# Performance work log

Measured on AMD Instinct MI355X. Metric: run time of the kernel, lower is better.

## Reference

```python
import jax, jax.numpy as jnp
import numpy as np

N = 100_000   # nodes
E = 1_600_000 # edges (avg degree 16)
IN, H, C = 3, 32, 4
DIMS = [(IN, H), (H, 2 * H), (2 * H, 3 * H), (3 * H, 4 * H)]  # SAGEConv layer dims


def setup_inputs() -> dict:
    key = jax.random.key(0)
    ks = jax.random.split(key, 16)
    inp = {
        "x": jax.random.normal(ks[0], (N, IN), dtype=jnp.float32),
        "edge_index": jax.random.randint(ks[1], (2, E), 0, N, dtype=jnp.int32).astype(jnp.int64),
    }
    i = 2
    for l, (din, dout) in enumerate(DIMS):
        s = 1.0 / float(np.sqrt(din))
        inp[f"Wl{l}"] = jax.random.normal(ks[i], (din, dout), dtype=jnp.float32) * s; i += 1
        inp[f"bl{l}"] = jnp.zeros((dout,), jnp.float32)
        inp[f"Wr{l}"] = jax.random.normal(ks[i], (din, dout), dtype=jnp.float32) * s; i += 1
    sf = 1.0 / float(np.sqrt(4 * H))
    inp["Wf"] = jax.random.normal(ks[i], (4 * H, C), dtype=jnp.float32) * sf
    inp["bf"] = jnp.zeros((C,), jnp.float32)
    return inp


def _sage_conv(h, src, dst, Wl, bl, Wr):
    # PyG SAGEConv (aggr='mean'): lin_l(mean_{j in N(i)} x_j) + lin_r(x_i)
    n = h.shape[0]
    agg = jax.ops.segment_sum(h[src], dst, num_segments=n)            # [N, din]
    deg = jax.ops.segment_sum(jnp.ones((src.shape[0],), h.dtype), dst, num_segments=n)
    mean = agg / jnp.maximum(deg, 1.0)[:, None]
    return mean @ Wl + bl + h @ Wr


def reference(x, edge_index, Wl0, bl0, Wr0, Wl1, bl1, Wr1, Wl2, bl2, Wr2, Wl3, bl3, Wr3, Wf, bf):
    src, dst = edge_index[0], edge_index[1]
    h = x
    for Wl, bl, Wr in ((Wl0, bl0, Wr0), (Wl1, bl1, Wr1), (Wl2, bl2, Wr2), (Wl3, bl3, Wr3)):
        h = jax.nn.relu(_sage_conv(h, src, dst, Wl, bl, Wr))
    return jax.nn.sigmoid(h @ Wf + bf)  # [N, class_num]
```

## Files before the change

### kernel.cpp

```cpp
#include <hip/hip_runtime.h>
#include <math.h>

#define NN 100000
#define NE 1600000
#define BUCKETS ((NN + 255) >> 8)
#define RTH 1024
#define RVPT 4

typedef short bf16x8 __attribute__((ext_vector_type(8)));
typedef float f32x4 __attribute__((ext_vector_type(4)));

__device__ inline float bsf(unsigned short u) { return __uint_as_float(((unsigned)u) << 16); }
__device__ inline unsigned short f2bs(float f) {
    unsigned u = __float_as_uint(f);
    return (unsigned short)((u + 0x7fffu + ((u >> 16) & 1u)) >> 16);
}

__global__ __launch_bounds__(RTH) void bhist_k(const int* __restrict__ dst,
                                               int* __restrict__ bhist) {
    __shared__ int bh[BUCKETS];
    for (int i = threadIdx.x; i < BUCKETS; i += RTH) bh[i] = 0;
    __syncthreads();
    int e0 = blockIdx.x * (RTH * RVPT) + threadIdx.x;
#pragma unroll
    for (int v = 0; v < RVPT; ++v) {
        int e = e0 + v * RTH;
        if (e < NE) atomicAdd(&bh[dst[e] >> 8], 1);
    }
    __syncthreads();
    for (int i = threadIdx.x; i < BUCKETS; i += RTH)
        if (bh[i]) atomicAdd(&bhist[i], bh[i]);
}

__global__ __launch_bounds__(512) void bscan_k(const int* __restrict__ bhist,
                                               int* __restrict__ bcur) {
    __shared__ int buf[512];
    int tid = threadIdx.x;
    int v = (tid < BUCKETS) ? bhist[tid] : 0;
    buf[tid] = v;
    __syncthreads();
    for (int off = 1; off < 512; off <<= 1) {
        int t = (tid >= off) ? buf[tid - off] : 0;
        __syncthreads();
        buf[tid] += t;
        __syncthreads();
    }
    if (tid < BUCKETS) bcur[tid] = buf[tid] - v;
}

__global__ __launch_bounds__(RTH) void reorder_k(const int* __restrict__ src,
                                                 const int* __restrict__ dst,
                                                 int* __restrict__ bcur,
                                                 unsigned long long* __restrict__ ebuf) {
    __shared__ int hist[BUCKETS];
    __shared__ int base[BUCKETS];
    int tid = threadIdx.x;
    for (int i = tid; i < BUCKETS; i += RTH) hist[i] = 0;
    __syncthreads();
    int e0 = blockIdx.x * (RTH * RVPT) + tid;
    unsigned long long pair[RVPT];
    int pr[RVPT];
#pragma unroll
    for (int v = 0; v < RVPT; ++v) {
        int e = e0 + v * RTH;
        if (e < NE) {
            int s = src[e], d = dst[e];
            pair[v] = ((unsigned long long)(unsigned)d << 32) | (unsigned)s;
            int b = d >> 8;
            int r = atomicAdd(&hist[b], 1);
            pr[v] = (b << 12) | r;
        } else pr[v] = -1;
    }
    __syncthreads();
    for (int i = tid; i < BUCKETS; i += RTH)
        base[i] = hist[i] ? atomicAdd(&bcur[i], hist[i]) : 0;
    __syncthreads();
#pragma unroll
    for (int v = 0; v < RVPT; ++v) {
        if (pr[v] >= 0) {
            int b = pr[v] >> 12, r = pr[v] & 4095;
            ebuf[(size_t)base[b] + r] = pair[v];
        }
    }
}

__global__ __launch_bounds__(512) void pcsr_k(const unsigned long long* __restrict__ ebuf,
                                              const int* __restrict__ bend,
                                              int* __restrict__ row_ptr,
                                              int* __restrict__ col) {
    __shared__ int hist[256];
    __shared__ int wsum[4];
    int b = blockIdx.x;
    int tid = threadIdx.x;
    int beg = b ? bend[b - 1] : 0;
    int end = bend[b];

    if (tid < 256) hist[tid] = 0;
    __syncthreads();
    for (int e = beg + tid; e < end; e += 512)
        atomicAdd(&hist[(int)(ebuf[e] >> 32) & 255], 1);
    __syncthreads();

    int v = 0, excl = 0;
    if (tid < 256) {
        v = hist[tid];
        int lane = tid & 63, wid = tid >> 6;
        int s = v;
#pragma unroll
        for (int off = 1; off < 64; off <<= 1) {
            int t = __shfl_up(s, off);
            if (lane >= off) s += t;
        }
        if (lane == 63) wsum[wid] = s;
        excl = s - v;
    }
    __syncthreads();
    if (tid < 256) {
        int wid = tid >> 6;
        int prev = 0;
#pragma unroll
        for (int w = 0; w < 4; ++w) prev += (w < wid) ? wsum[w] : 0;
        excl += beg + prev;
        int node = b * 256 + tid;
        if (node < NN) row_ptr[node] = excl;
        if (node == NN - 1) row_ptr[NN] = excl + v;
    }
    __syncthreads();
    if (tid < 256) hist[tid] = excl;
    __syncthreads();
    for (int e = beg + tid; e < end; e += 512) {
        unsigned long long p = ebuf[e];
        int d = (int)(p >> 32);
        int pos = atomicAdd(&hist[d & 255], 1);
        col[pos] = (int)(p & 0xffffffffu);
    }
}

__global__ __launch_bounds__(256) void wcvt_all_k(
    const float* __restrict__ Wl1, const float* __restrict__ Wr1,
    const float* __restrict__ Wl2, const float* __restrict__ Wr2,
    const float* __restrict__ Wl3, const float* __restrict__ Wr3,
    unsigned short* __restrict__ wt1, unsigned short* __restrict__ wt2,
    unsigned short* __restrict__ wt3) {
    int idx = blockIdx.x * 256 + threadIdx.x;
    if (idx < 4096) {
        int j = idx >> 6, k = idx & 63;
        float v = (k < 32) ? Wl1[k * 64 + j] : Wr1[(k - 32) * 64 + j];
        wt1[idx] = f2bs(v);
    } else if (idx < 16384) {
        int t = idx - 4096;
        int j = t / 128, k = t - j * 128;
        float v = (k < 64) ? Wl2[k * 96 + j] : Wr2[(k - 64) * 96 + j];
        wt2[t] = f2bs(v);
    } else if (idx < 40960) {
        int t = idx - 16384;
        int j = t / 192, k = t - j * 192;
        float v = (k < 96) ? Wl3[k * 128 + j] : Wr3[(k - 96) * 128 + j];
        wt3[t] = f2bs(v);
    }
}

__global__ __launch_bounds__(256) void agg0_k(const int* __restrict__ rp, const int* __restrict__ col,
                                              const float* __restrict__ x, unsigned short* __restrict__ magg) {
    int node = blockIdx.x * 4 + (threadIdx.x >> 6);
    int lane = threadIdx.x & 63;
    int fl = lane & 3, es = lane >> 2;
    int beg = rp[node], end = rp[node + 1];
    float acc = 0.0f;
    for (int e = beg + es; e < end; e += 16) {
        unsigned off = (unsigned)(col[e] * 3);
        if (fl < 3) acc += x[off + fl];
    }
    acc += __shfl(acc, lane + 32);
    acc += __shfl(acc, lane + 16);
    acc += __shfl(acc, lane + 8);
    acc += __shfl(acc, lane + 4);
    if (lane < 3) {
        float inv = 1.0f / fmaxf((float)(end - beg), 1.0f);
        magg[(size_t)node * 3 + lane] = f2bs(acc * inv);
    }
}

template<int DIN, int FL, int EPW>
__global__ __launch_bounds__(256) void agg_k(const int* __restrict__ rp, const int* __restrict__ col,
                                             const unsigned short* __restrict__ hb,
                                             unsigned short* __restrict__ magg) {
    int node = blockIdx.x * 4 + (threadIdx.x >> 6);
    int lane = threadIdx.x & 63;
    int fl = lane % FL;
    int es = lane / FL;
    int beg = rp[node], end = rp[node + 1];

    float a[8];
#pragma unroll
    for (int i = 0; i < 8; ++i) a[i] = 0.0f;

    if (es < EPW) {
        for (int e = beg + es; e < end; e += 4 * EPW) {
            int e1 = e + EPW, e2 = e + 2 * EPW, e3 = e + 3 * EPW;
            bool b1 = e1 < end, b2 = e2 < end, b3 = e3 < end;
            unsigned o0 = (unsigned)(col[e] * DIN);
            unsigned o1 = (unsigned)(col[b1 ? e1 : e] * DIN);
            unsigned o2 = (unsigned)(col[b2 ? e2 : e] * DIN);
            unsigned o3 = (unsigned)(col[b3 ? e3 : e] * DIN);
            uint4 v0 = *(const uint4*)(hb + o0 + fl * 8);
            uint4 v1 = *(const uint4*)(hb + o1 + fl * 8);
            uint4 v2 = *(const uint4*)(hb + o2 + fl * 8);
            uint4 v3 = *(const uint4*)(hb + o3 + fl * 8);
            float m1 = b1 ? 1.0f : 0.0f;
            float m2 = b2 ? 1.0f : 0.0f;
            float m3 = b3 ? 1.0f : 0.0f;
            const unsigned short* p0 = (const unsigned short*)&v0;
            const unsigned short* p1 = (const unsigned short*)&v1;
            const unsigned short* p2 = (const unsigned short*)&v2;
            const unsigned short* p3 = (const unsigned short*)&v3;
#pragma unroll
            for (int i = 0; i < 8; ++i) {
                a[i] += bsf(p0[i]);
                a[i] = fmaf(bsf(p1[i]), m1, a[i]);
                a[i] = fmaf(bsf(p2[i]), m2, a[i]);
                a[i] = fmaf(bsf(p3[i]), m3, a[i]);
            }
        }
    }

    if constexpr (FL == 4) {
#pragma unroll
        for (int i = 0; i < 8; ++i) {
            a[i] += __shfl(a[i], lane + 4);
            a[i] += __shfl(a[i], lane + 8);
            a[i] += __shfl(a[i], lane + 16);
            a[i] += __shfl(a[i], lane + 32);
        }
    } else if constexpr (FL == 8) {
#pragma unroll
        for (int i = 0; i < 8; ++i) {
            a[i] += __shfl(a[i], lane + 8);
            a[i] += __shfl(a[i], lane + 16);
            a[i] += __shfl(a[i], lane + 32);
        }
    } else {
#pragma unroll
        for (int i = 0; i < 8; ++i) {
            float g4 = __shfl(a[i], lane + 48);
            a[i] += __shfl(a[i], lane + 12);
            a[i] += __shfl(a[i], lane + 24);
            a[i] += g4;
        }
    }

    if (lane < FL) {
        float inv = 1.0f / fmaxf((float)(end - beg), 1.0f);
        unsigned short o[8];
#pragma unroll
        for (int i = 0; i < 8; ++i) o[i] = f2bs(a[i] * inv);
        *(uint4*)(magg + (size_t)node * DIN + fl * 8) = *(const uint4*)o;
    }
}

template<int DIN, int DOUT, int CT>
__global__ __launch_bounds__(256) void gemm_k(
    const unsigned short* __restrict__ magg, const float* __restrict__ hx,
    const float* __restrict__ Wl, const float* __restrict__ bl, const float* __restrict__ Wr,
    unsigned short* __restrict__ hout)
{
    __shared__ float sm[32][DIN + 1];
    __shared__ float sh[32][DIN + 1];

    int tx = threadIdx.x;
    int base = blockIdx.x * 32;

    for (int f = tx; f < 32 * 3; f += 256) {
        int n = f / 3, k = f - n * 3;
        sm[n][k] = bsf(magg[(size_t)(base + n) * 3 + k]);
        sh[n][k] = hx[(size_t)(base + n) * 3 + k];
    }
    __syncthreads();

    int ng = tx >> 5, cg = tx & 31;
    float acc[4][CT];
#pragma unroll
    for (int m = 0; m < 4; ++m)
#pragma unroll
        for (int c = 0; c < CT; ++c) acc[m][c] = bl[cg * CT + c];

#pragma unroll
    for (int k = 0; k < 3; ++k) {
        float wl[CT], wr[CT];
#pragma unroll
        for (int c = 0; c < CT; ++c) {
            wl[c] = Wl[(size_t)k * DOUT + cg * CT + c];
            wr[c] = Wr[(size_t)k * DOUT + cg * CT + c];
        }
#pragma unroll
        for (int m = 0; m < 4; ++m) {
            float mv = sm[ng * 4 + m][k];
            float hv = sh[ng * 4 + m][k];
#pragma unroll
            for (int c = 0; c < CT; ++c)
                acc[m][c] = fmaf(mv, wl[c], fmaf(hv, wr[c], acc[m][c]));
        }
    }

#pragma unroll
    for (int m = 0; m < 4; ++m)
#pragma unroll
        for (int c = 0; c < CT; ++c) {
            float v = fmaxf(acc[m][c], 0.0f);
            hout[(size_t)(base + ng * 4 + m) * DOUT + cg * CT + c] = f2bs(v);
        }
}

template<int DIN, int DOUT, bool FINAL>
__global__ __launch_bounds__(256) void mgemm_k(
    const unsigned short* __restrict__ magg, const unsigned short* __restrict__ h,
    const unsigned short* __restrict__ Wt, const float* __restrict__ bl,
    const float* __restrict__ Wf, const float* __restrict__ bfi,
    unsigned short* __restrict__ hout, float* __restrict__ out)
{
    constexpr int K2  = 2 * DIN;
    constexpr int STR = K2 + 8;
    constexpr int NT  = DOUT / 16;
    constexpr int KS  = K2 / 32;
    __shared__ unsigned short lA[64 * STR];
    __shared__ unsigned short lB[DOUT * STR];

    int tx = threadIdx.x;
    int base = blockIdx.x * 64;

    constexpr int CPM = DIN / 8;
    for (int c = tx; c < 64 * CPM; c += 256) {
        int n = c / CPM, o = (c - n * CPM) * 8;
        int node = base + n;
        uint4 vm = make_uint4(0, 0, 0, 0), vh = vm;
        if (node < NN) {
            vm = *(const uint4*)(magg + (size_t)node * DIN + o);
            vh = *(const uint4*)(h    + (size_t)node * DIN + o);
        }
        *(uint4*)(lA + n * STR + o)       = vm;
        *(uint4*)(lA + n * STR + DIN + o) = vh;
    }
    constexpr int CPW = K2 / 8;
    for (int c = tx; c < DOUT * CPW; c += 256) {
        int j = c / CPW, o = (c - j * CPW) * 8;
        *(uint4*)(lB + j * STR + o) = *(const uint4*)(Wt + (size_t)j * K2 + o);
    }
    __syncthreads();

    int lane = tx & 63;
    int wm = tx >> 6;
    int r16 = lane & 15, kg = lane >> 4;

    f32x4 acc[NT];
#pragma unroll
    for (int t = 0; t < NT; ++t) acc[t] = (f32x4){0.0f, 0.0f, 0.0f, 0.0f};

#pragma unroll
    for (int kk = 0; kk < KS; ++kk) {
        bf16x8 a = *(const bf16x8*)(lA + (wm * 16 + r16) * STR + kk * 32 + kg * 8);
#pragma unroll
        for (int t = 0; t < NT; ++t) {
            bf16x8 b = *(const bf16x8*)(lB + (t * 16 + r16) * STR + kk * 32 + kg * 8);
            acc[t] = __builtin_amdgcn_mfma_f32_16x16x32_bf16(a, b, acc[t], 0, 0, 0);
        }
    }

    if (!FINAL) {
#pragma unroll
        for (int t = 0; t < NT; ++t)
#pragma unroll
            for (int r = 0; r < 4; ++r) {
                int node = base + wm * 16 + kg * 4 + r;
                int colj = t * 16 + r16;
                float v = fmaxf(acc[t][r] + bl[colj], 0.0f);
                if (node < NN) hout[(size_t)node * DOUT + colj] = f2bs(v);
            }
    } else {
        __syncthreads();
        float* s4 = (float*)lB;
#pragma unroll
        for (int t = 0; t < NT; ++t)
#pragma unroll
            for (int r = 0; r < 4; ++r) {
                int nl = wm * 16 + kg * 4 + r;
                int colj = t * 16 + r16;
                s4[nl * 129 + colj] = fmaxf(acc[t][r] + bl[colj], 0.0f);
            }
        __syncthreads();
        int nl = tx >> 2, c = tx & 3;
        int node = base + nl;
        if (node < NN) {
            float a = bfi[c];
#pragma unroll 8
            for (int k = 0; k < 128; ++k)
                a = fmaf(s4[nl * 129 + k], Wf[k * 4 + c], a);
            out[(size_t)node * 4 + c] = 1.0f / (1.0f + expf(-a));
        }
    }
}

extern "C" void kernel_launch(void* const* d_in, const int* in_sizes, int n_in,
                              void* d_out, int out_size, void* d_ws, size_t ws_size,
                              hipStream_t stream) {
    const float* x   = (const float*)d_in[0];
    const int*   ei  = (const int*)d_in[1];
    const int*   src = ei;
    const int*   dst = ei + NE;
    const float* Wl0 = (const float*)d_in[2];
    const float* bl0 = (const float*)d_in[3];
    const float* Wr0 = (const float*)d_in[4];
    const float* Wl1 = (const float*)d_in[5];
    const float* bl1 = (const float*)d_in[6];
    const float* Wr1 = (const float*)d_in[7];
    const float* Wl2 = (const float*)d_in[8];
    const float* bl2 = (const float*)d_in[9];
    const float* Wr2 = (const float*)d_in[10];
    const float* Wl3 = (const float*)d_in[11];
    const float* bl3 = (const float*)d_in[12];
    const float* Wr3 = (const float*)d_in[13];
    const float* Wf  = (const float*)d_in[14];
    const float* bf  = (const float*)d_in[15];
    float* out = (float*)d_out;

    size_t ints = (size_t)(NN + 2) + 512 + 512 + NE;
    ints = (ints + 15) & ~(size_t)15;
    size_t need = ints * 4 + (size_t)NN * (96 + 32 + 64 + 96) * 2
                + (size_t)(64 * 64 + 96 * 128 + 128 * 192) * 2;
    if (ws_size < need) return;

    int* row_ptr = (int*)d_ws;
    int* bhist   = row_ptr + NN + 2;
    int* bcur    = bhist + 512;
    int* col     = bcur + 512;
    unsigned short* magg = (unsigned short*)((char*)d_ws + ints * 4);
    unsigned long long* ebuf = (unsigned long long*)magg;
    unsigned short* h1   = magg + (size_t)NN * 96;
    unsigned short* h2   = h1 + (size_t)NN * 32;
    unsigned short* h3   = h2 + (size_t)NN * 64;
    unsigned short* wt1  = h3 + (size_t)NN * 96;
    unsigned short* wt2  = wt1 + 64 * 64;
    unsigned short* wt3  = wt2 + 96 * 128;

    wcvt_all_k<<<160, 256, 0, stream>>>(Wl1, Wr1, Wl2, Wr2, Wl3, Wr3, wt1, wt2, wt3);

    hipMemsetAsync(bhist, 0, 512 * sizeof(int), stream);
    const int EB = (NE + RTH * RVPT - 1) / (RTH * RVPT);
    bhist_k<<<EB, RTH, 0, stream>>>(dst, bhist);
    bscan_k<<<1, 512, 0, stream>>>(bhist, bcur);
    reorder_k<<<EB, RTH, 0, stream>>>(src, dst, bcur, ebuf);
    pcsr_k<<<BUCKETS, 512, 0, stream>>>(ebuf, bcur, row_ptr, col);

    const int AGRID = NN / 4;
    const int MG    = (NN + 63) / 64;

    agg0_k<<<AGRID, 256, 0, stream>>>(row_ptr, col, x, magg);
    gemm_k<3, 32, 1><<<NN / 32, 256, 0, stream>>>(magg, x, Wl0, bl0, Wr0, h1);

    agg_k<32, 4, 16><<<AGRID, 256, 0, stream>>>(row_ptr, col, h1, magg);
    mgemm_k<32, 64, false><<<MG, 256, 0, stream>>>(
        magg, h1, wt1, bl1, nullptr, nullptr, h2, nullptr);

    agg_k<64, 8, 8><<<AGRID, 256, 0, stream>>>(row_ptr, col, h2, magg);
    mgemm_k<64, 96, false><<<MG, 256, 0, stream>>>(
        magg, h2, wt2, bl2, nullptr, nullptr, h3, nullptr);

    agg_k<96, 12, 5><<<AGRID, 256, 0, stream>>>(row_ptr, col, h3, magg);
    mgemm_k<96, 128, true><<<MG, 256, 0, stream>>>(
        magg, h3, wt3, bl3, Wf, bf, nullptr, out);
}
```

Baseline: 289.1 us.

## Fuse neighbor aggregation into MFMA GEMM kernels and reduce final layer in registers

Merges the per-layer mean-aggregation kernel into the MFMA GEMM kernel, so each block aggregates its 64 nodes straight into shared memory. This removes the aggregated-feature round trip through global memory and one launch per layer. Weight tiles are no longer staged in LDS but read from global memory (cache) inside the MFMA loop. The final classifier is now reduced with cross-lane shuffles instead of an LDS pass. The risk is lower parallelism: each wave now walks 16 nodes serially, and the grid shrinks from 25000 blocks to about 1563.

Result: slower. 341.5 us (+18.1%).

```diff
diff --git a/kernel.cpp b/kernel.cpp
--- a/kernel.cpp
+++ b/kernel.cpp
@@ -181,83 +181,6 @@
     }
 }
 
-template<int DIN, int FL, int EPW>
-__global__ __launch_bounds__(256) void agg_k(const int* __restrict__ rp, const int* __restrict__ col,
-                                             const unsigned short* __restrict__ hb,
-                                             unsigned short* __restrict__ magg) {
-    int node = blockIdx.x * 4 + (threadIdx.x >> 6);
-    int lane = threadIdx.x & 63;
-    int fl = lane % FL;
-    int es = lane / FL;
-    int beg = rp[node], end = rp[node + 1];
-
-    float a[8];
-#pragma unroll
-    for (int i = 0; i < 8; ++i) a[i] = 0.0f;
-
-    if (es < EPW) {
-        for (int e = beg + es; e < end; e += 4 * EPW) {
-            int e1 = e + EPW, e2 = e + 2 * EPW, e3 = e + 3 * EPW;
-            bool b1 = e1 < end, b2 = e2 < end, b3 = e3 < end;
-            unsigned o0 = (unsigned)(col[e] * DIN);
-            unsigned o1 = (unsigned)(col[b1 ? e1 : e] * DIN);
-            unsigned o2 = (unsigned)(col[b2 ? e2 : e] * DIN);
-            unsigned o3 = (unsigned)(col[b3 ? e3 : e] * DIN);
-            uint4 v0 = *(const uint4*)(hb + o0 + fl * 8);
-            uint4 v1 = *(const uint4*)(hb + o1 + fl * 8);
-            uint4 v2 = *(const uint4*)(hb + o2 + fl * 8);
-            uint4 v3 = *(const uint4*)(hb + o3 + fl * 8);
-            float m1 = b1 ? 1.0f : 0.0f;
-            float m2 = b2 ? 1.0f : 0.0f;
-            float m3 = b3 ? 1.0f : 0.0f;
-            const unsigned short* p0 = (const unsigned short*)&v0;
-            const unsigned short* p1 = (const unsigned short*)&v1;
-            const unsigned short* p2 = (const unsigned short*)&v2;
-            const unsigned short* p3 = (const unsigned short*)&v3;
-#pragma unroll
-            for (int i = 0; i < 8; ++i) {
-                a[i] += bsf(p0[i]);
-                a[i] = fmaf(bsf(p1[i]), m1, a[i]);
-                a[i] = fmaf(bsf(p2[i]), m2, a[i]);
-                a[i] = fmaf(bsf(p3[i]), m3, a[i]);
-            }
-        }
-    }
-
-    if constexpr (FL == 4) {
-#pragma unroll
-        for (int i = 0; i < 8; ++i) {
-            a[i] += __shfl(a[i], lane + 4);
-            a[i] += __shfl(a[i], lane + 8);
-            a[i] += __shfl(a[i], lane + 16);
-            a[i] += __shfl(a[i], lane + 32);
-        }
-    } else if constexpr (FL == 8) {
-#pragma unroll
-        for (int i = 0; i < 8; ++i) {
-            a[i] += __shfl(a[i], lane + 8);
-            a[i] += __shfl(a[i], lane + 16);
-            a[i] += __shfl(a[i], lane + 32);
-        }
-    } else {
-#pragma unroll
-        for (int i = 0; i < 8; ++i) {
-            float g4 = __shfl(a[i], lane + 48);
-            a[i] += __shfl(a[i], lane + 12);
-            a[i] += __shfl(a[i], lane + 24);
-            a[i] += g4;
-        }
-    }
-
-    if (lane < FL) {
-        float inv = 1.0f / fmaxf((float)(end - beg), 1.0f);
-        unsigned short o[8];
-#pragma unroll
-        for (int i = 0; i < 8; ++i) o[i] = f2bs(a[i] * inv);
-        *(uint4*)(magg + (size_t)node * DIN + fl * 8) = *(const uint4*)o;
-    }
-}
-
 template<int DIN, int DOUT, int CT>
 __global__ __launch_bounds__(256) void gemm_k(
     const unsigned short* __restrict__ magg, const float* __restrict__ hx,
@@ -312,8 +235,9 @@
 }
 
 template<int DIN, int DOUT, bool FINAL>
-__global__ __launch_bounds__(256) void mgemm_k(
-    const unsigned short* __restrict__ magg, const unsigned short* __restrict__ h,
+__global__ __launch_bounds__(256) void fused_k(
+    const int* __restrict__ rp, const int* __restrict__ col,
+    const unsigned short* __restrict__ h,
     const unsigned short* __restrict__ Wt, const float* __restrict__ bl,
     const float* __restrict__ Wf, const float* __restrict__ bfi,
     unsigned short* __restrict__ hout, float* __restrict__ out)
@@ -322,33 +246,100 @@
     constexpr int STR = K2 + 8;
     constexpr int NT  = DOUT / 16;
     constexpr int KS  = K2 / 32;
+    constexpr int FL  = DIN / 8;
+    constexpr int EPW = 64 / FL;
     __shared__ unsigned short lA[64 * STR];
-    __shared__ unsigned short lB[DOUT * STR];
 
     int tx = threadIdx.x;
+    int lane = tx & 63;
+    int wm = tx >> 6;
     int base = blockIdx.x * 64;
 
     constexpr int CPM = DIN / 8;
     for (int c = tx; c < 64 * CPM; c += 256) {
         int n = c / CPM, o = (c - n * CPM) * 8;
         int node = base + n;
-        uint4 vm = make_uint4(0, 0, 0, 0), vh = vm;
-        if (node < NN) {
-            vm = *(const uint4*)(magg + (size_t)node * DIN + o);
-            vh = *(const uint4*)(h    + (size_t)node * DIN + o);
-        }
-        *(uint4*)(lA + n * STR + o)       = vm;
+        uint4 vh = make_uint4(0, 0, 0, 0);
+        if (node < NN) vh = *(const uint4*)(h + (size_t)node * DIN + o);
         *(uint4*)(lA + n * STR + DIN + o) = vh;
     }
-    constexpr int CPW = K2 / 8;
-    for (int c = tx; c < DOUT * CPW; c += 256) {
-        int j = c / CPW, o = (c - j * CPW) * 8;
-        *(uint4*)(lB + j * STR + o) = *(const uint4*)(Wt + (size_t)j * K2 + o);
-    }
-    __syncthreads();
-
-    int lane = tx & 63;
-    int wm = tx >> 6;
+
+    int fl = lane % FL;
+    int es = lane / FL;
+    for (int i = 0; i < 16; ++i) {
+        int n = wm * 16 + i;
+        int node = base + n;
+        int beg = 0, end = 0;
+        if (node < NN) { beg = rp[node]; end = rp[node + 1]; }
+
+        float a[8];
+#pragma unroll
+        for (int j = 0; j < 8; ++j) a[j] = 0.0f;
+
+        if (es < EPW) {
+            for (int e = beg + es; e < end; e += 4 * EPW) {
+                int e1 = e + EPW, e2 = e + 2 * EPW, e3 = e + 3 * EPW;
+                bool b1 = e1 < end, b2 = e2 < end, b3 = e3 < end;
+                unsigned o0 = (unsigned)(col[e] * DIN);
+                unsigned o1 = (unsigned)(col[b1 ? e1 : e] * DIN);
+                unsigned o2 = (unsigned)(col[b2 ? e2 : e] * DIN);
+                unsigned o3 = (unsigned)(col[b3 ? e3 : e] * DIN);
+                uint4 v0 = *(const uint4*)(h + o0 + fl * 8);
+                uint4 v1 = *(const uint4*)(h + o1 + fl * 8);
+                uint4 v2 = *(const uint4*)(h + o2 + fl * 8);
+                uint4 v3 = *(const uint4*)(h + o3 + fl * 8);
+                float m1 = b1 ? 1.0f : 0.0f;
+                float m2 = b2 ? 1.0f : 0.0f;
+                float m3 = b3 ? 1.0f : 0.0f;
+                const unsigned short* p0 = (const unsigned short*)&v0;
+                const unsigned short* p1 = (const unsigned short*)&v1;
+                const unsigned short* p2 = (const unsigned short*)&v2;
+                const unsigned short* p3 = (const unsigned short*)&v3;
+#pragma unroll
+                for (int j = 0; j < 8; ++j) {
+                    a[j] += bsf(p0[j]);
+                    a[j] = fmaf(bsf(p1[j]), m1, a[j]);
+                    a[j] = fmaf(bsf(p2[j]), m2, a[j]);
+                    a[j] = fmaf(bsf(p3[j]), m3, a[j]);
+                }
+            }
+        }
+
+        if constexpr (FL == 4) {
+#pragma unroll
+            for (int j = 0; j < 8; ++j) {
+                a[j] += __shfl(a[j], lane + 4);
+                a[j] += __shfl(a[j], lane + 8);
+                a[j] += __shfl(a[j], lane + 16);
+                a[j] += __shfl(a[j], lane + 32);
+            }
+        } else if constexpr (FL == 8) {
+#pragma unroll
+            for (int j = 0; j < 8; ++j) {
+                a[j] += __shfl(a[j], lane + 8);
+                a[j] += __shfl(a[j], lane + 16);
+                a[j] += __shfl(a[j], lane + 32);
+            }
+        } else {
+#pragma unroll
+            for (int j = 0; j < 8; ++j) {
+                float g4 = __shfl(a[j], lane + 48);
+                a[j] += __shfl(a[j], lane + 12);
+                a[j] += __shfl(a[j], lane + 24);
+                a[j] += g4;
+            }
+        }
+
+        if (lane < FL) {
+            float inv = 1.0f / fmaxf((float)(end - beg), 1.0f);
+            unsigned short o8[8];
+#pragma unroll
+            for (int j = 0; j < 8; ++j) o8[j] = f2bs(a[j] * inv);
+            *(uint4*)(lA + n * STR + fl * 8) = *(const uint4*)o8;
+        }
+    }
+    __syncthreads();
+
     int r16 = lane & 15, kg = lane >> 4;
 
     f32x4 acc[NT];
@@ -360,7 +351,7 @@
         bf16x8 a = *(const bf16x8*)(lA + (wm * 16 + r16) * STR + kk * 32 + kg * 8);
 #pragma unroll
         for (int t = 0; t < NT; ++t) {
-            bf16x8 b = *(const bf16x8*)(lB + (t * 16 + r16) * STR + kk * 32 + kg * 8);
+            bf16x8 b = *(const bf16x8*)(Wt + (size_t)(t * 16 + r16) * K2 + kk * 32 + kg * 8);
             acc[t] = __builtin_amdgcn_mfma_f32_16x16x32_bf16(a, b, acc[t], 0, 0, 0);
         }
     }
@@ -376,25 +367,42 @@
                 if (node < NN) hout[(size_t)node * DOUT + colj] = f2bs(v);
             }
     } else {
-        __syncthreads();
-        float* s4 = (float*)lB;
-#pragma unroll
-        for (int t = 0; t < NT; ++t)
+        float p[4][4];
+#pragma unroll
+        for (int r = 0; r < 4; ++r)
+#pragma unroll
+            for (int c = 0; c < 4; ++c) p[r][c] = 0.0f;
+#pragma unroll
+        for (int t = 0; t < NT; ++t) {
+            int colj = t * 16 + r16;
+            float bv = bl[colj];
 #pragma unroll
             for (int r = 0; r < 4; ++r) {
-                int nl = wm * 16 + kg * 4 + r;
-                int colj = t * 16 + r16;
-                s4[nl * 129 + colj] = fmaxf(acc[t][r] + bl[colj], 0.0f);
-            }
-        __syncthreads();
-        int nl = tx >> 2, c = tx & 3;
-        int node = base + nl;
-        if (node < NN) {
-            float a = bfi[c];
-#pragma unroll 8
-            for (int k = 0; k < 128; ++k)
-                a = fmaf(s4[nl * 129 + k], Wf[k * 4 + c], a);
-            out[(size_t)node * 4 + c] = 1.0f / (1.0f + expf(-a));
+                float v = fmaxf(acc[t][r] + bv, 0.0f);
+#pragma unroll
+                for (int c = 0; c < 4; ++c)
+                    p[r][c] = fmaf(v, Wf[colj * 4 + c], p[r][c]);
+            }
+        }
+#pragma unroll
+        for (int r = 0; r < 4; ++r)
+#pragma unroll
+            for (int c = 0; c < 4; ++c) {
+                p[r][c] += __shfl_xor(p[r][c], 1);
+                p[r][c] += __shfl_xor(p[r][c], 2);
+                p[r][c] += __shfl_xor(p[r][c], 4);
+                p[r][c] += __shfl_xor(p[r][c], 8);
+            }
+        if (r16 == 0) {
+#pragma unroll
+            for (int r = 0; r < 4; ++r) {
+                int node = base + wm * 16 + kg * 4 + r;
+                if (node < NN) {
+#pragma unroll
+                    for (int c = 0; c < 4; ++c)
+                        out[(size_t)node * 4 + c] = 1.0f / (1.0f + expf(-(p[r][c] + bfi[c])));
+                }
+            }
         }
     }
 }
@@ -450,21 +458,17 @@
     reorder_k<<<EB, RTH, 0, stream>>>(src, dst, bcur, ebuf);
     pcsr_k<<<BUCKETS, 512, 0, stream>>>(ebuf, bcur, row_ptr, col);
 
-    const int AGRID = NN / 4;
-    const int MG    = (NN + 63) / 64;
-
-    agg0_k<<<AGRID, 256, 0, stream>>>(row_ptr, col, x, magg);
+    const int MG = (NN + 63) / 64;
+
+    agg0_k<<<NN / 4, 256, 0, stream>>>(row_ptr, col, x, magg);
     gemm_k<3, 32, 1><<<NN / 32, 256, 0, stream>>>(magg, x, Wl0, bl0, Wr0, h1);
 
-    agg_k<32, 4, 16><<<AGRID, 256, 0, stream>>>(row_ptr, col, h1, magg);
-    mgemm_k<32, 64, false><<<MG, 256, 0, stream>>>(
-        magg, h1, wt1, bl1, nullptr, nullptr, h2, nullptr);
-
-    agg_k<64, 8, 8><<<AGRID, 256, 0, stream>>>(row_ptr, col, h2, magg);
-    mgemm_k<64, 96, false><<<MG, 256, 0, stream>>>(
-        magg, h2, wt2, bl2, nullptr, nullptr, h3, nullptr);
-
-    agg_k<96, 12, 5><<<AGRID, 256, 0, stream>>>(row_ptr, col, h3, magg);
-    mgemm_k<96, 128, true><<<MG, 256, 0, stream>>>(
-        magg, h3, wt3, bl3, Wf, bf, nullptr, out);
-}
+    fused_k<32, 64, false><<<MG, 256, 0, stream>>>(
+        row_ptr, col, h1, wt1, bl1, nullptr, nullptr, h2, nullptr);
+
+    fused_k<64, 96, false><<<MG, 256, 0, stream>>>(
+        row_ptr, col, h2, wt2, bl2, nullptr, nullptr, h3, nullptr);
+
+    fused_k<96, 128, true><<<MG, 256, 0, stream>>>(
+        row_ptr, col, h3, wt3, bl3, Wf, bf, nullptr, out);
+}
```
